# Performance work log

Measured on AMD Instinct MI355X. Metric: run time of the kernel, lower is better.

## Reference

```python
import jax, jax.numpy as jnp
import numpy as np

D_MODEL = 1024
NUM_HEADS = 16
DFF = 4096
LN_EPS = 1e-08
CLIP = 10.0


def setup_inputs() -> dict:
    key = jax.random.key(0)
    ks = jax.random.split(key, 12)
    d, h, f = D_MODEL, NUM_HEADS, DFF
    s = 1.0 / np.sqrt(d)
    inp = {
        "x": jax.random.normal(ks[0], (4, 2048, d), dtype=jnp.float32),
        "wq": jax.random.normal(ks[1], (d, d), dtype=jnp.float32) * s,
        "bq": jnp.zeros((d,), jnp.float32),
        "wk": jax.random.normal(ks[2], (d, d), dtype=jnp.float32) * s,
        "bk": jnp.zeros((d,), jnp.float32),
        "wv": jax.random.normal(ks[3], (d, d), dtype=jnp.float32) * s,
        "bv": jnp.zeros((d,), jnp.float32),
        "wo": jax.random.normal(ks[4], (d, d), dtype=jnp.float32) * s,
        "bo": jnp.zeros((d,), jnp.float32),
        "w1": jax.random.normal(ks[5], (d, f), dtype=jnp.float32) * s,
        "b1": jnp.zeros((f,), jnp.float32),
        "w2": jax.random.normal(ks[6], (f, d), dtype=jnp.float32) * (1.0 / np.sqrt(f)),
        "b2": jnp.zeros((d,), jnp.float32),
        "ln_gamma": jnp.ones((d,), jnp.float32),
        "ln_beta": jnp.zeros((d,), jnp.float32),
    }
    return inp


def layernorm(x, gamma, beta):
    mu = jnp.mean(x, axis=-1, keepdims=True)
    var = jnp.var(x, axis=-1, keepdims=True)
    return (x - mu) * jax.lax.rsqrt(var + LN_EPS) * gamma + beta


def encoder_layer(x, wq, bq, wk, bk, wv, bv, wo, bo, w1, b1, w2, b2, ln_gamma, ln_beta):
    B, S, d = x.shape
    H = NUM_HEADS
    Dh = d // H
    q = (x @ wq + bq).reshape(B, S, H, Dh).transpose(0, 2, 1, 3)  # bhsd
    k = (x @ wk + bk).reshape(B, S, H, Dh).transpose(0, 2, 1, 3)
    v = (x @ wv + bv).reshape(B, S, H, Dh).transpose(0, 2, 1, 3)
    logits = jnp.einsum('bhqd,bhkd->bhqk', q, k) / jnp.sqrt(jnp.float32(Dh))
    logits = jnp.clip(logits, -CLIP, CLIP)
    attn = jax.nn.softmax(logits, axis=-1)
    ctx = jnp.einsum('bhqk,bhkd->bhqd', attn, v)
    ctx = ctx.transpose(0, 2, 1, 3).reshape(B, S, d)
    attn_out = ctx @ wo + bo
    out1 = layernorm(x + attn_out, ln_gamma, ln_beta)
    ffn = jax.nn.relu(out1 @ w1 + b1) @ w2 + b2
    return layernorm(out1 + ffn, ln_gamma, ln_beta)


def reference(x, wq, bq, wk, bk, wv, bv, wo, bo, w1, b1, w2, b2, ln_gamma, ln_beta):
    return encoder_layer(x, wq, bq, wk, bk, wv, bv, wo, bo, w1, b1, w2, b2, ln_gamma, ln_beta)
```

## Files before the change

kernel.cpp:

```cpp
#include <hip/hip_runtime.h>
#include <stdint.h>

#define D_MODEL 1024
#define NHEAD 16
#define DH 64
#define DFF 4096
#define BATCH 4
#define SEQ 2048
#define MTOT (BATCH*SEQ)

#define QSCALE 0.18033688011112043f
#define CLIP2  14.426950408889634f

typedef short short8 __attribute__((ext_vector_type(8)));
typedef float f32x4 __attribute__((ext_vector_type(4)));
typedef unsigned int uint;

__device__ inline unsigned short f2bf(float f) {
  union { float f; unsigned u; } v; v.f = f;
  unsigned r = v.u + 0x7fffu + ((v.u >> 16) & 1u);
  return (unsigned short)(r >> 16);
}
__device__ inline float bf2f(unsigned short b) {
  union { unsigned u; float f; } v; v.u = ((unsigned)b) << 16;
  return v.f;
}
__device__ inline unsigned pack_trunc(float lo, float hi) {
  union { float f; unsigned u; } a, b; a.f = lo; b.f = hi;
  return __builtin_amdgcn_perm(b.u, a.u, 0x07060302u);
}
__device__ __forceinline__ void async16(const unsigned short* g, unsigned short* l) {
  __builtin_amdgcn_global_load_lds(
      (const __attribute__((address_space(1))) unsigned int*)g,
      (__attribute__((address_space(3))) unsigned int*)l, 16, 0, 0);
}

__global__ void cast_kernel(const float* __restrict__ in, unsigned short* __restrict__ out, int n4) {
  int i = blockIdx.x * blockDim.x + threadIdx.x;
  if (i < n4) {
    float4 v = ((const float4*)in)[i];
    ushort4 o;
    o.x = f2bf(v.x); o.y = f2bf(v.y); o.z = f2bf(v.z); o.w = f2bf(v.w);
    ((ushort4*)out)[i] = o;
  }
}

__global__ void transpose_weights_kernel(
    const float* __restrict__ wq, const float* __restrict__ wk,
    const float* __restrict__ wv, const float* __restrict__ wo,
    const float* __restrict__ w1, const float* __restrict__ w2,
    unsigned short* __restrict__ wqkvT, unsigned short* __restrict__ woT,
    unsigned short* __restrict__ w1T, unsigned short* __restrict__ w2T) {
  __shared__ __align__(16) unsigned short tile[64][72];
  const int id = blockIdx.x;
  const float* in; unsigned short* out; int K, N, n0, k0; float scale = 1.0f;
  if (id < 1024) {
    const int wi = id >> 8, t = id & 255;
    switch (wi) {
      case 0:  in = wq; out = wqkvT;           scale = QSCALE; break;
      case 1:  in = wk; out = wqkvT + 1048576; break;
      case 2:  in = wv; out = wqkvT + 2097152; break;
      default: in = wo; out = woT;             break;
    }
    K = 1024; N = 1024; n0 = (t & 15) * 64; k0 = (t >> 4) * 64;
  } else if (id < 2048) {
    const int t = id - 1024;
    in = w1; out = w1T; K = 1024; N = 4096; n0 = (t & 63) * 64; k0 = (t >> 6) * 64;
  } else {
    const int t = id - 2048;
    in = w2; out = w2T; K = 4096; N = 1024; n0 = (t & 15) * 64; k0 = (t >> 4) * 64;
  }
  const int tx = threadIdx.x & 15, ty = threadIdx.x >> 4;
#pragma unroll
  for (int j = 0; j < 64; j += 16) {
    float4 v = *(const float4*)(in + (size_t)(k0 + ty + j) * N + n0 + tx * 4);
    tile[tx * 4 + 0][ty + j] = f2bf(v.x * scale);
    tile[tx * 4 + 1][ty + j] = f2bf(v.y * scale);
    tile[tx * 4 + 2][ty + j] = f2bf(v.z * scale);
    tile[tx * 4 + 3][ty + j] = f2bf(v.w * scale);
  }
  __syncthreads();
  const int r = threadIdx.x >> 3, c = threadIdx.x & 7;
#pragma unroll
  for (int j = 0; j < 64; j += 32)
    *(uint4*)(out + (size_t)(n0 + r + j) * K + k0 + c * 8) =
        *(const uint4*)(&tile[r + j][c * 8]);
}

__global__ void bias_concat_kernel(const float* __restrict__ bq, const float* __restrict__ bk,
                                   const float* __restrict__ bv, float* __restrict__ o) {
  int i = blockIdx.x * 256 + threadIdx.x;
  if (i < 3 * D_MODEL) {
    float v = (i < D_MODEL) ? bq[i] * QSCALE
            : (i < 2 * D_MODEL) ? bk[i - D_MODEL] : bv[i - 2 * D_MODEL];
    o[i] = v;
  }
}

__global__ void transpose_v_kernel(const unsigned short* __restrict__ QKV,
                                   unsigned short* __restrict__ Vt) {
  __shared__ unsigned short tile[32][33];
  int bh = blockIdx.z, b = bh >> 4, h = bh & 15;
  int kv0 = blockIdx.x * 32, dh0 = blockIdx.y * 32;
  int tx = threadIdx.x & 31, ty = threadIdx.x >> 5;
#pragma unroll
  for (int j = 0; j < 32; j += 8)
    tile[ty + j][tx] = QKV[(size_t)(b * SEQ + kv0 + ty + j) * 3072 + 2048 + h * DH + dh0 + tx];
  __syncthreads();
#pragma unroll
  for (int j = 0; j < 32; j += 8)
    Vt[(size_t)(bh * DH + dh0 + ty + j) * SEQ + kv0 + tx] = tile[tx][ty + j];
}

#define MFMA_Q(mh, nh)                                                                     \
  _Pragma("unroll")                                                                        \
  for (int ks = 0; ks < 2; ks++) {                                                         \
    _Pragma("unroll")                                                                      \
    for (int i = 0; i < 4; i++) {                                                          \
      _Pragma("unroll")                                                                    \
      for (int nn = 0; nn < 2; nn++) {                                                     \
        acc[(mh)*4 + i][(nh)*2 + nn] = __builtin_amdgcn_mfma_f32_16x16x32_bf16(            \
            af[i][ks], bf[(nh)*2 + nn][ks], acc[(mh)*4 + i][(nh)*2 + nn], 0, 0, 0);        \
      }                                                                                    \
    }                                                                                      \
  }

template<int RELU, int OUT_BF16, int KSPLIT, int BIAS>
__global__ __launch_bounds__(512, 2) void gemm256_bt_kernel(
    const unsigned short* __restrict__ A,
    const unsigned short* __restrict__ Bt,
    const float* __restrict__ bias,
    void* __restrict__ Cout,
    int M, int N, int K) {
  __shared__ __align__(16) unsigned short lds[65536];

  const int nwg = gridDim.x;
  int nid = (blockIdx.x & 7) * (nwg >> 3) + (blockIdx.x >> 3);
  int kh = 0;
  if (KSPLIT == 2) { kh = nid & 1; nid >>= 1; }
  const int GX = N >> 8;
  const int im = nid / GX, in_ = nid % GX;
  const int m0 = im * 256, n0 = in_ * 256;

  const int tid = threadIdx.x;
  const int lane = tid & 63, wave = tid >> 6;
  const int wm = (wave >> 2) * 128, wn = (wave & 3) * 64;
  const int lm = lane & 15, lg = lane >> 4;
  const int rot = lm & 7;
  const int aoff0 = ((lg) ^ rot) << 3;
  const int aoff1 = ((4 + lg) ^ rot) << 3;
  const int arow = (wm + lm) << 6;
  const int brow = (wn + lm) << 6;

  const int kbeg = (KSPLIT == 2) ? kh * (K >> 1) : 0;
  const int nk = ((KSPLIT == 2) ? (K >> 1) : K) >> 6;

  const int rb = tid >> 3;
  const int gcol = (((tid & 7) ^ (rb & 7)) << 3);
  const unsigned short* gA = A  + (size_t)(m0 + rb) * K + kbeg + gcol;
  const unsigned short* gB = Bt + (size_t)(n0 + rb) * K + kbeg + gcol;

  auto stage = [&](const unsigned short* g, int b, int st, unsigned short* seg) {
    async16(g + (size_t)b * 64 * K + (size_t)st * 64, seg + b * 4096 + tid * 8);
  };

  f32x4 acc[8][4] = {};

  {
    unsigned short* A0s = lds;
    unsigned short* B0s = lds + 16384;
    unsigned short* A1s = lds + 32768;
    unsigned short* B1s = lds + 49152;
    stage(gA, 0, 0, A0s); stage(gA, 2, 0, A0s);
    stage(gB, 0, 0, B0s); stage(gB, 1, 0, B0s);
    stage(gA, 1, 0, A0s); stage(gA, 3, 0, A0s);
    stage(gB, 2, 0, B0s); stage(gB, 3, 0, B0s);
    stage(gA, 0, 1, A1s); stage(gA, 2, 1, A1s);
    stage(gB, 0, 1, B1s); stage(gB, 1, 1, B1s);
    stage(gA, 1, 1, A1s); stage(gA, 3, 1, A1s);
    __builtin_amdgcn_s_waitcnt(0x0F76);
    __builtin_amdgcn_s_barrier();
  }

  for (int t = 0; t < nk; ++t) {
    const int cur = t & 1;
    unsigned short* LA = lds + (cur << 15);
    unsigned short* LB = LA + 16384;
    unsigned short* NA = lds + ((cur ^ 1) << 15);
    unsigned short* NB = NA + 16384;
    short8 af[4][2], bf[4][2];

    if (t + 1 < nk) { stage(gB, 2, t + 1, NB); stage(gB, 3, t + 1, NB); }
#pragma unroll
    for (int i = 0; i < 4; i++) {
      af[i][0] = *(const short8*)(LA + arow + i * 1024 + aoff0);
      af[i][1] = *(const short8*)(LA + arow + i * 1024 + aoff1);
    }
#pragma unroll
    for (int n = 0; n < 2; n++) {
      bf[n][0] = *(const short8*)(LB + brow + n * 1024 + aoff0);
      bf[n][1] = *(const short8*)(LB + brow + n * 1024 + aoff1);
    }
    __builtin_amdgcn_s_barrier();
    __builtin_amdgcn_s_setprio(1);
    MFMA_Q(0, 0);
    __builtin_amdgcn_s_setprio(0);
    __builtin_amdgcn_s_barrier();

    if (t + 2 < nk) { stage(gA, 0, t + 2, LA); stage(gA, 2, t + 2, LA); }
#pragma unroll
    for (int n = 2; n < 4; n++) {
      bf[n][0] = *(const short8*)(LB + brow + n * 1024 + aoff0);
      bf[n][1] = *(const short8*)(LB + brow + n * 1024 + aoff1);
    }
    __builtin_amdgcn_s_barrier();
    __builtin_amdgcn_s_setprio(1);
    MFMA_Q(0, 1);
    __builtin_amdgcn_s_setprio(0);
    __builtin_amdgcn_s_barrier();

    if (t + 2 < nk) { stage(gB, 0, t + 2, LB); stage(gB, 1, t + 2, LB); }
#pragma unroll
    for (int i = 0; i < 4; i++) {
      af[i][0] = *(const short8*)(LA + arow + 4096 + i * 1024 + aoff0);
      af[i][1] = *(const short8*)(LA + arow + 4096 + i * 1024 + aoff1);
    }
    __builtin_amdgcn_s_barrier();
    __builtin_amdgcn_s_setprio(1);
    MFMA_Q(1, 1);
    __builtin_amdgcn_s_setprio(0);
    __builtin_amdgcn_s_barrier();

    if (t + 2 < nk) {
      stage(gA, 1, t + 2, LA); stage(gA, 3, t + 2, LA);
      __builtin_amdgcn_s_waitcnt(0x0F76);
    } else {
      __builtin_amdgcn_s_waitcnt(0x0F70);
    }
    __builtin_amdgcn_s_barrier();
    __builtin_amdgcn_s_setprio(1);
    MFMA_Q(1, 0);
    __builtin_amdgcn_s_setprio(0);
    __builtin_amdgcn_s_barrier();
  }

  unsigned short* Cb = (unsigned short*)Cout + (KSPLIT == 2 ? (size_t)kh * M * N : 0);
#pragma unroll
  for (int nt = 0; nt < 4; nt++) {
    int col = n0 + wn + nt * 16 + lm;
    float bv = BIAS ? bias[col] : 0.0f;
#pragma unroll
    for (int mf = 0; mf < 8; mf++) {
#pragma unroll
      for (int r = 0; r < 4; r++) {
        int row = m0 + wm + mf * 16 + lg * 4 + r;
        float v = acc[mf][nt][r] + bv;
        if (RELU) v = fmaxf(v, 0.0f);
        if (OUT_BF16) Cb[(size_t)row * N + col] = f2bf(v);
        else          ((float*)Cout)[(size_t)row * N + col] = v;
      }
    }
  }
}

__global__ __launch_bounds__(512, 4) void attn_kernel(
    const unsigned short* __restrict__ QKV,
    const unsigned short* __restrict__ Vt_g,
    unsigned short* __restrict__ ctx) {
  __shared__ __align__(16) unsigned short Ks[2][4096];
  __shared__ __align__(16) unsigned short Vs[2][4096];
  __shared__ __align__(16) unsigned short Ps[8 * 2048];
  const int bh = blockIdx.x, b = bh >> 4, h = bh & 15;
  const int q0 = blockIdx.y * 256;
  const int tid = threadIdx.x, wave = tid >> 6, lane = tid & 63;
  const int lm = lane & 15, lq = lane >> 4;
  const int rot = (lm & 7) * 8;

  short8 qf[2][2];
#pragma unroll
  for (int ntq = 0; ntq < 2; ntq++) {
    const unsigned short* qp =
        QKV + (size_t)(b * SEQ + q0 + wave * 32 + ntq * 16 + lm) * 3072 + h * DH;
#pragma unroll
    for (int sl = 0; sl < 2; sl++) qf[ntq][sl] = *(const short8*)(qp + sl * 32 + lq * 8);
  }
  const short8 ones = {0x3F80, 0x3F80, 0x3F80, 0x3F80, 0x3F80, 0x3F80, 0x3F80, 0x3F80};
  f32x4 oacc[2][4] = {};
  f32x4 lsum[2] = {};

  const int srow = tid >> 3;
  const int ssl = (tid & 7) ^ (srow & 7);
  const unsigned short* kg =
      QKV + (size_t)(b * SEQ + srow) * 3072 + D_MODEL + h * DH + ssl * 8;
  const unsigned short* vg = Vt_g + (size_t)(bh * DH + srow) * SEQ + ssl * 8;
  unsigned short* kdst = &Ks[0][0] + tid * 8;
  unsigned short* vdst = &Vs[0][0] + tid * 8;

  async16(kg, kdst);
  async16(vg, vdst);

  for (int it = 0; it < SEQ / 64; it++) {
    const int buf = it & 1;
    __builtin_amdgcn_s_waitcnt(0x0F70);
    __builtin_amdgcn_s_barrier();
    __builtin_amdgcn_sched_barrier(0);
    if (it + 1 < SEQ / 64) {
      const int nb = (buf ^ 1) * 4096;
      async16(kg + (size_t)(it + 1) * 64 * 3072, kdst + nb);
      async16(vg + (it + 1) * 64, vdst + nb);
    }
    const unsigned short* Kb = &Ks[buf][0];
    const unsigned short* Vb = &Vs[buf][0];

#pragma unroll
    for (int mt = 0; mt < 4; mt++) {
      const unsigned short* krow = Kb + (mt * 16 + lm) * 64;
      short8 kf0 = *(const short8*)(krow + ((lq * 8) ^ rot));
      short8 kf1 = *(const short8*)(krow + ((32 + lq * 8) ^ rot));
#pragma unroll
      for (int ntq = 0; ntq < 2; ntq++) {
        f32x4 sa = {0.f, 0.f, 0.f, 0.f};
        __builtin_amdgcn_s_setprio(1);
        sa = __builtin_amdgcn_mfma_f32_16x16x32_bf16(kf0, qf[ntq][0], sa, 0, 0, 0);
        sa = __builtin_amdgcn_mfma_f32_16x16x32_bf16(kf1, qf[ntq][1], sa, 0, 0, 0);
        __builtin_amdgcn_s_setprio(0);
        float p0 = exp2f(fminf(sa[0], CLIP2));
        float p1 = exp2f(fminf(sa[1], CLIP2));
        float p2 = exp2f(fminf(sa[2], CLIP2));
        float p3 = exp2f(fminf(sa[3], CLIP2));
        uint2 d;
        d.x = pack_trunc(p0, p1);
        d.y = pack_trunc(p2, p3);
        *(uint2*)(Ps + wave * 2048 + (ntq * 16 + lm) * 64 + ((mt * 16 + lq * 4) ^ rot)) = d;
      }
    }
    __builtin_amdgcn_s_waitcnt(0xC07F);
    short8 pf[2][2];
#pragma unroll
    for (int mq = 0; mq < 2; mq++)
#pragma unroll
      for (int sl = 0; sl < 2; sl++)
        pf[mq][sl] = *(const short8*)(Ps + wave * 2048 + (mq * 16 + lm) * 64 + ((sl * 32 + lq * 8) ^ rot));
    __builtin_amdgcn_s_setprio(1);
#pragma unroll
    for (int nt = 0; nt < 4; nt++) {
      const unsigned short* vrow = Vb + (nt * 16 + lm) * 64;
      short8 vf0 = *(const short8*)(vrow + ((lq * 8) ^ rot));
      short8 vf1 = *(const short8*)(vrow + ((32 + lq * 8) ^ rot));
#pragma unroll
      for (int mq = 0; mq < 2; mq++) {
        oacc[mq][nt] = __builtin_amdgcn_mfma_f32_16x16x32_bf16(pf[mq][0], vf0, oacc[mq][nt], 0, 0, 0);
        oacc[mq][nt] = __builtin_amdgcn_mfma_f32_16x16x32_bf16(pf[mq][1], vf1, oacc[mq][nt], 0, 0, 0);
      }
    }
#pragma unroll
    for (int mq = 0; mq < 2; mq++) {
      lsum[mq] = __builtin_amdgcn_mfma_f32_16x16x32_bf16(pf[mq][0], ones, lsum[mq], 0, 0, 0);
      lsum[mq] = __builtin_amdgcn_mfma_f32_16x16x32_bf16(pf[mq][1], ones, lsum[mq], 0, 0, 0);
    }
    __builtin_amdgcn_s_setprio(0);
  }

#pragma unroll
  for (int mq = 0; mq < 2; mq++) {
    float linv[4];
#pragma unroll
    for (int r = 0; r < 4; r++) linv[r] = 1.0f / lsum[mq][r];
    const size_t rowbase =
        (size_t)(b * SEQ + q0 + wave * 32 + mq * 16 + lq * 4) * D_MODEL + h * DH;
#pragma unroll
    for (int nt = 0; nt < 4; nt++) {
#pragma unroll
      for (int r = 0; r < 4; r++) {
        ctx[rowbase + (size_t)r * D_MODEL + nt * 16 + lm] = f2bf(oacc[mq][nt][r] * linv[r]);
      }
    }
  }
}

template<int B_BF16, int WRITE_BF16, int THREE>
__global__ void ln_kernel(const float* __restrict__ A, const void* __restrict__ Bv,
                          const void* __restrict__ B2v, const float* __restrict__ cbias,
                          const float* __restrict__ gamma, const float* __restrict__ beta,
                          float* __restrict__ outf, unsigned short* __restrict__ outb) {
  const int row = blockIdx.x;
  const int tid = threadIdx.x;
  const size_t base = (size_t)row * D_MODEL + tid * 4;
  float4 xa = *(const float4*)(A + base);
  float4 xb;
  if (B_BF16) {
    ushort4 u = *(const ushort4*)((const unsigned short*)Bv + base);
    xb.x = bf2f(u.x); xb.y = bf2f(u.y); xb.z = bf2f(u.z); xb.w = bf2f(u.w);
  } else {
    xb = *(const float4*)((const float*)Bv + base);
  }
  if (THREE) {
    ushort4 u2 = *(const ushort4*)((const unsigned short*)B2v + base);
    float4 cb = *(const float4*)(cbias + tid * 4);
    xb.x += bf2f(u2.x) + cb.x; xb.y += bf2f(u2.y) + cb.y;
    xb.z += bf2f(u2.z) + cb.z; xb.w += bf2f(u2.w) + cb.w;
  }
  float v0 = xa.x + xb.x, v1 = xa.y + xb.y, v2 = xa.z + xb.z, v3 = xa.w + xb.w;
  float s = v0 + v1 + v2 + v3;
  float sq = v0 * v0 + v1 * v1 + v2 * v2 + v3 * v3;
#pragma unroll
  for (int off = 1; off < 64; off <<= 1) {
    s  += __shfl_xor(s, off);
    sq += __shfl_xor(sq, off);
  }
  __shared__ float red[8];
  int wave = tid >> 6;
  if ((tid & 63) == 0) { red[wave * 2] = s; red[wave * 2 + 1] = sq; }
  __syncthreads();
  s  = red[0] + red[2] + red[4] + red[6];
  sq = red[1] + red[3] + red[5] + red[7];
  float mean = s * (1.0f / D_MODEL);
  float var = sq * (1.0f / D_MODEL) - mean * mean;
  float inv = rsqrtf(var + 1e-8f);
  float4 g  = *(const float4*)(gamma + tid * 4);
  float4 be = *(const float4*)(beta + tid * 4);
  float o0 = (v0 - mean) * inv * g.x + be.x;
  float o1 = (v1 - mean) * inv * g.y + be.y;
  float o2 = (v2 - mean) * inv * g.z + be.z;
  float o3 = (v3 - mean) * inv * g.w + be.w;
  float4 of; of.x = o0; of.y = o1; of.z = o2; of.w = o3;
  *(float4*)(outf + base) = of;
  if (WRITE_BF16) {
    ushort4 ub; ub.x = f2bf(o0); ub.y = f2bf(o1); ub.z = f2bf(o2); ub.w = f2bf(o3);
    *(ushort4*)(outb + base) = ub;
  }
}

extern "C" void kernel_launch(void* const* d_in, const int* in_sizes, int n_in,
                              void* d_out, int out_size, void* d_ws, size_t ws_size,
                              hipStream_t stream) {
  const float* x     = (const float*)d_in[0];
  const float* wq    = (const float*)d_in[1];
  const float* bq    = (const float*)d_in[2];
  const float* wk    = (const float*)d_in[3];
  const float* bk    = (const float*)d_in[4];
  const float* wv    = (const float*)d_in[5];
  const float* bv    = (const float*)d_in[6];
  const float* wo    = (const float*)d_in[7];
  const float* bo    = (const float*)d_in[8];
  const float* w1    = (const float*)d_in[9];
  const float* b1    = (const float*)d_in[10];
  const float* w2    = (const float*)d_in[11];
  const float* b2    = (const float*)d_in[12];
  const float* gamma = (const float*)d_in[13];
  const float* beta  = (const float*)d_in[14];

  char* ws = (char*)d_ws;
  const size_t MB = 1ull << 20;
  unsigned short* xb      = (unsigned short*)(ws + 0 * MB);
  unsigned short* out1b   = (unsigned short*)(ws + 0 * MB);
  unsigned short* ffn2    = (unsigned short*)(ws + 0 * MB);
  unsigned short* wqkvT   = (unsigned short*)(ws + 16 * MB);
  unsigned short* woT     = (unsigned short*)(ws + 22 * MB);
  unsigned short* w1T     = (unsigned short*)(ws + 24 * MB);
  unsigned short* w2T     = (unsigned short*)(ws + 32 * MB);
  float*          bqkv    = (float*)(ws + 40 * MB);
  unsigned short* qkvb    = (unsigned short*)(ws + 41 * MB);
  unsigned short* oprojp  = (unsigned short*)(ws + 41 * MB);
  unsigned short* h1      = (unsigned short*)(ws + 41 * MB);
  unsigned short* Vt_g    = (unsigned short*)(ws + 89 * MB);
  unsigned short* ctx     = (unsigned short*)(ws + 105 * MB);
  float*          out1f   = (float*)(ws + 121 * MB);

  cast_kernel<<<(MTOT * D_MODEL / 4 + 255) / 256, 256, 0, stream>>>(x, xb, MTOT * D_MODEL / 4);
  transpose_weights_kernel<<<3072, 256, 0, stream>>>(
      wq, wk, wv, wo, w1, w2, wqkvT, woT, w1T, w2T);
  bias_concat_kernel<<<12, 256, 0, stream>>>(bq, bk, bv, bqkv);

  gemm256_bt_kernel<0, 1, 1, 1><<<(3072 / 256) * (MTOT / 256), 512, 0, stream>>>(
      xb, wqkvT, bqkv, qkvb, MTOT, 3072, D_MODEL);
  transpose_v_kernel<<<dim3(SEQ / 32, DH / 32, BATCH * NHEAD), 256, 0, stream>>>(qkvb, Vt_g);
  attn_kernel<<<dim3(BATCH * NHEAD, SEQ / 256), 512, 0, stream>>>(qkvb, Vt_g, ctx);

  gemm256_bt_kernel<0, 1, 2, 0><<<2 * (D_MODEL / 256) * (MTOT / 256), 512, 0, stream>>>(
      ctx, woT, nullptr, oprojp, MTOT, D_MODEL, D_MODEL);
  ln_kernel<1, 1, 1><<<MTOT, 256, 0, stream>>>(
      x, oprojp, oprojp + (size_t)MTOT * D_MODEL, bo, gamma, beta, out1f, out1b);
  gemm256_bt_kernel<1, 1, 1, 1><<<(DFF / 256) * (MTOT / 256), 512, 0, stream>>>(
      out1b, w1T, b1, h1, MTOT, DFF, D_MODEL);
  gemm256_bt_kernel<0, 1, 2, 0><<<2 * (D_MODEL / 256) * (MTOT / 256), 512, 0, stream>>>(
      h1, w2T, nullptr, ffn2, MTOT, D_MODEL, DFF);
  ln_kernel<1, 0, 1><<<MTOT, 256, 0, stream>>>(
      out1f, ffn2, ffn2 + (size_t)MTOT * D_MODEL, b2, gamma, beta, (float*)d_out, nullptr);
}
```

Before: 541.5 us.

## Restructure attention to 256-thread blocks with register-staged K/V prefetch

The attention kernel moves from 512-thread blocks covering 256 queries to 256-thread blocks covering 128 queries, which doubles the grid. The async global-to-LDS double buffer becomes register prefetch into a single LDS buffer, with two __syncthreads per KV tile. It also replaces exp2f with the hardware exp2 builtin and drops the setprio hints. Smaller blocks and less LDS are meant to raise occupancy, at the cost of extra barriers and more K/V reloads from global memory.

```diff
diff --git a/kernel.cpp b/kernel.cpp
--- a/kernel.cpp
+++ b/kernel.cpp
@@ -28,6 +28,9 @@
 __device__ inline unsigned pack_trunc(float lo, float hi) {
   union { float f; unsigned u; } a, b; a.f = lo; b.f = hi;
   return __builtin_amdgcn_perm(b.u, a.u, 0x07060302u);
+}
+__device__ __forceinline__ float hw_exp2(float x) {
+  return __builtin_amdgcn_exp2f(x);
 }
 __device__ __forceinline__ void async16(const unsigned short* g, unsigned short* l) {
   __builtin_amdgcn_global_load_lds(
@@ -263,17 +266,18 @@
   }
 }
 
-__global__ __launch_bounds__(512, 4) void attn_kernel(
+__global__ __launch_bounds__(256, 4) void attn_kernel(
     const unsigned short* __restrict__ QKV,
     const unsigned short* __restrict__ Vt_g,
     unsigned short* __restrict__ ctx) {
-  __shared__ __align__(16) unsigned short Ks[2][4096];
-  __shared__ __align__(16) unsigned short Vs[2][4096];
-  __shared__ __align__(16) unsigned short Ps[8 * 2048];
+  __shared__ __align__(16) unsigned short Ks[64 * 64];
+  __shared__ __align__(16) unsigned short Vs[64 * 64];
+  __shared__ __align__(16) unsigned short Ps[4 * 32 * 64];
   const int bh = blockIdx.x, b = bh >> 4, h = bh & 15;
-  const int q0 = blockIdx.y * 256;
+  const int q0 = blockIdx.y * 128;
   const int tid = threadIdx.x, wave = tid >> 6, lane = tid & 63;
   const int lm = lane & 15, lq = lane >> 4;
+  const int srow = tid >> 3, scol = (tid & 7) * 8;
   const int rot = (lm & 7) * 8;
 
   short8 qf[2][2];
@@ -288,46 +292,43 @@
   f32x4 oacc[2][4] = {};
   f32x4 lsum[2] = {};
 
-  const int srow = tid >> 3;
-  const int ssl = (tid & 7) ^ (srow & 7);
-  const unsigned short* kg =
-      QKV + (size_t)(b * SEQ + srow) * 3072 + D_MODEL + h * DH + ssl * 8;
-  const unsigned short* vg = Vt_g + (size_t)(bh * DH + srow) * SEQ + ssl * 8;
-  unsigned short* kdst = &Ks[0][0] + tid * 8;
-  unsigned short* vdst = &Vs[0][0] + tid * 8;
-
-  async16(kg, kdst);
-  async16(vg, vdst);
+  const int sdst = srow * 64 + (scol ^ ((srow & 7) * 8));
+  const unsigned short* kg = QKV + (size_t)(b * SEQ) * 3072 + D_MODEL + h * DH + scol;
+  const unsigned short* vg = Vt_g + (size_t)(bh * DH + srow) * SEQ + scol;
+
+  uint4 kr0 = *(const uint4*)(kg + (size_t)srow * 3072);
+  uint4 kr1 = *(const uint4*)(kg + (size_t)(srow + 32) * 3072);
+  uint4 vr0 = *(const uint4*)(vg);
+  uint4 vr1 = *(const uint4*)(vg + 32 * SEQ);
 
   for (int it = 0; it < SEQ / 64; it++) {
-    const int buf = it & 1;
-    __builtin_amdgcn_s_waitcnt(0x0F70);
-    __builtin_amdgcn_s_barrier();
-    __builtin_amdgcn_sched_barrier(0);
+    *(uint4*)(Ks + sdst)        = kr0;
+    *(uint4*)(Ks + sdst + 2048) = kr1;
+    *(uint4*)(Vs + sdst)        = vr0;
+    *(uint4*)(Vs + sdst + 2048) = vr1;
+    __syncthreads();
     if (it + 1 < SEQ / 64) {
-      const int nb = (buf ^ 1) * 4096;
-      async16(kg + (size_t)(it + 1) * 64 * 3072, kdst + nb);
-      async16(vg + (it + 1) * 64, vdst + nb);
-    }
-    const unsigned short* Kb = &Ks[buf][0];
-    const unsigned short* Vb = &Vs[buf][0];
+      const int kvn = (it + 1) * 64;
+      kr0 = *(const uint4*)(kg + (size_t)(kvn + srow) * 3072);
+      kr1 = *(const uint4*)(kg + (size_t)(kvn + srow + 32) * 3072);
+      vr0 = *(const uint4*)(vg + kvn);
+      vr1 = *(const uint4*)(vg + 32 * SEQ + kvn);
+    }
 
 #pragma unroll
     for (int mt = 0; mt < 4; mt++) {
-      const unsigned short* krow = Kb + (mt * 16 + lm) * 64;
+      const unsigned short* krow = Ks + (mt * 16 + lm) * 64;
       short8 kf0 = *(const short8*)(krow + ((lq * 8) ^ rot));
       short8 kf1 = *(const short8*)(krow + ((32 + lq * 8) ^ rot));
 #pragma unroll
       for (int ntq = 0; ntq < 2; ntq++) {
         f32x4 sa = {0.f, 0.f, 0.f, 0.f};
-        __builtin_amdgcn_s_setprio(1);
         sa = __builtin_amdgcn_mfma_f32_16x16x32_bf16(kf0, qf[ntq][0], sa, 0, 0, 0);
         sa = __builtin_amdgcn_mfma_f32_16x16x32_bf16(kf1, qf[ntq][1], sa, 0, 0, 0);
-        __builtin_amdgcn_s_setprio(0);
-        float p0 = exp2f(fminf(sa[0], CLIP2));
-        float p1 = exp2f(fminf(sa[1], CLIP2));
-        float p2 = exp2f(fminf(sa[2], CLIP2));
-        float p3 = exp2f(fminf(sa[3], CLIP2));
+        float p0 = hw_exp2(fminf(sa[0], CLIP2));
+        float p1 = hw_exp2(fminf(sa[1], CLIP2));
+        float p2 = hw_exp2(fminf(sa[2], CLIP2));
+        float p3 = hw_exp2(fminf(sa[3], CLIP2));
         uint2 d;
         d.x = pack_trunc(p0, p1);
         d.y = pack_trunc(p2, p3);
@@ -341,10 +342,9 @@
 #pragma unroll
       for (int sl = 0; sl < 2; sl++)
         pf[mq][sl] = *(const short8*)(Ps + wave * 2048 + (mq * 16 + lm) * 64 + ((sl * 32 + lq * 8) ^ rot));
-    __builtin_amdgcn_s_setprio(1);
 #pragma unroll
     for (int nt = 0; nt < 4; nt++) {
-      const unsigned short* vrow = Vb + (nt * 16 + lm) * 64;
+      const unsigned short* vrow = Vs + (nt * 16 + lm) * 64;
       short8 vf0 = *(const short8*)(vrow + ((lq * 8) ^ rot));
       short8 vf1 = *(const short8*)(vrow + ((32 + lq * 8) ^ rot));
 #pragma unroll
@@ -358,7 +358,7 @@
       lsum[mq] = __builtin_amdgcn_mfma_f32_16x16x32_bf16(pf[mq][0], ones, lsum[mq], 0, 0, 0);
       lsum[mq] = __builtin_amdgcn_mfma_f32_16x16x32_bf16(pf[mq][1], ones, lsum[mq], 0, 0, 0);
     }
-    __builtin_amdgcn_s_setprio(0);
+    __syncthreads();
   }
 
 #pragma unroll
@@ -475,7 +475,7 @@
   gemm256_bt_kernel<0, 1, 1, 1><<<(3072 / 256) * (MTOT / 256), 512, 0, stream>>>(
       xb, wqkvT, bqkv, qkvb, MTOT, 3072, D_MODEL);
   transpose_v_kernel<<<dim3(SEQ / 32, DH / 32, BATCH * NHEAD), 256, 0, stream>>>(qkvb, Vt_g);
-  attn_kernel<<<dim3(BATCH * NHEAD, SEQ / 256), 512, 0, stream>>>(qkvb, Vt_g, ctx);
+  attn_kernel<<<dim3(BATCH * NHEAD, SEQ / 128), 256, 0, stream>>>(qkvb, Vt_g, ctx);
 
   gemm256_bt_kernel<0, 1, 2, 0><<<2 * (D_MODEL / 256) * (MTOT / 256), 512, 0, stream>>>(
       ctx, woT, nullptr, oprojp, MTOT, D_MODEL, D_MODEL);
```

After: 530.7 us. 1.02x faster.
